# Kernel optimization log

Measured on AMD Instinct MI355X. Metric: run time of the kernel, lower is better.

Reference implementation:

```python
import jax, jax.numpy as jnp
import numpy as np

LN_EPS = 1e-5


def setup_inputs() -> dict:
    key = jax.random.key(0)
    kA, kX, kh = jax.random.split(key, 3)
    B, N, Cin, C, K = 16, 1024, 64, 64, 3
    A = jax.random.normal(kA, (B, N, N), dtype=jnp.float32)
    X = jax.random.normal(kX, (B, N, Cin), dtype=jnp.float32)
    h = jax.random.normal(kh, (K + 1, C, N), dtype=jnp.float32)
    ln_gamma = jnp.ones((C,), dtype=jnp.float32)
    ln_beta = jnp.zeros((C,), dtype=jnp.float32)
    return {"A": A, "X": X, "h": h, "ln_gamma": ln_gamma, "ln_beta": ln_beta}


def reference(A, X, h, ln_gamma, ln_beta):
    # Original loops compute, for each output channel c:
    #   sum_i sum_ch diag(h[i,c]) @ A^i @ X[..., ch]
    # which equals sum_i h[i,c,:] * (A^i @ X.sum(-1)).
    num_terms = h.shape[0] - 1  # static
    Xs = X.sum(-1)  # [B, N]
    powers = [Xs]
    p = Xs
    for _ in range(num_terms):  # static small loop over polynomial terms
        p = jnp.einsum('bnm,bm->bn', A, p)  # A^i @ Xs, matrix-vector per batch
        powers.append(p)
    P = jnp.stack(powers)  # [K+1, B, N]
    # node-variant per-channel taps: Y[b,n,c] = sum_i h[i,c,n] * P[i,b,n]
    Y = jnp.einsum('icn,ibn->bnc', h, P)  # [B, N, C]
    mu = Y.mean(axis=-1, keepdims=True)
    var = Y.var(axis=-1, keepdims=True)
    Yn = (Y - mu) / jnp.sqrt(var + LN_EPS) * ln_gamma + ln_beta
    return jnp.tanh(Yn)
```

## Files before the change

### kernel.cpp

```cpp
#include <hip/hip_runtime.h>
#include <math.h>

constexpr int B = 16, N = 1024, Cin = 64, C = 64, K = 3;
#define LN_EPS 1e-5f

__global__ void __launch_bounds__(256) k_front(const float* __restrict__ X,
                                               const float* __restrict__ h,
                                               float* __restrict__ P,
                                               float* __restrict__ ht) {
    __shared__ float tile[64 * 65];
    const int tid  = threadIdx.x;
    const int lane = tid & 63;
    const int w    = tid >> 6;
    const int gw   = blockIdx.x * 4 + w;

    for (int p = gw; p < B * N; p += 4096) {
        float v = X[(size_t)p * Cin + lane];
        #pragma unroll
        for (int off = 32; off; off >>= 1) v += __shfl_xor(v, off);
        if (lane == 0) P[p] = v;
    }

    if (blockIdx.x < (K + 1) * (N / 64)) {
        int i  = blockIdx.x / (N / 64);
        int n0 = (blockIdx.x % (N / 64)) * 64;
        const float* hi = h + (size_t)i * C * N;
        #pragma unroll
        for (int cc = w; cc < 64; cc += 4)
            tile[cc * 65 + lane] = hi[(size_t)cc * N + n0 + lane];
        __syncthreads();
        float* hti = ht + (size_t)i * N * C;
        #pragma unroll
        for (int nn = w; nn < 64; nn += 4)
            hti[(size_t)(n0 + nn) * C + lane] = tile[lane * 65 + nn];
    }
}

__device__ __forceinline__ void matvec4(const float* __restrict__ Ab,
                                        const float4* __restrict__ xs,
                                        int row, int lane,
                                        float& a0, float& a1, float& a2, float& a3) {
    const float4* r0 = (const float4*)(Ab + (size_t)(row + 0) * N);
    const float4* r1 = (const float4*)(Ab + (size_t)(row + 1) * N);
    const float4* r2 = (const float4*)(Ab + (size_t)(row + 2) * N);
    const float4* r3 = (const float4*)(Ab + (size_t)(row + 3) * N);
    a0 = a1 = a2 = a3 = 0.f;
    #pragma unroll
    for (int k = 0; k < 4; ++k) {
        int idx = k * 64 + lane;
        float4 xx = xs[idx];
        float4 v0 = r0[idx];
        float4 v1 = r1[idx];
        float4 v2 = r2[idx];
        float4 v3 = r3[idx];
        a0 += v0.x * xx.x + v0.y * xx.y + v0.z * xx.z + v0.w * xx.w;
        a1 += v1.x * xx.x + v1.y * xx.y + v1.z * xx.z + v1.w * xx.w;
        a2 += v2.x * xx.x + v2.y * xx.y + v2.z * xx.z + v2.w * xx.w;
        a3 += v3.x * xx.x + v3.y * xx.y + v3.z * xx.z + v3.w * xx.w;
    }
    #pragma unroll
    for (int off = 32; off; off >>= 1) {
        a0 += __shfl_xor(a0, off);
        a1 += __shfl_xor(a1, off);
        a2 += __shfl_xor(a2, off);
        a3 += __shfl_xor(a3, off);
    }
}

__global__ void __launch_bounds__(256) k_matvec(const float* __restrict__ A,
                                                const float* __restrict__ x,
                                                float* __restrict__ y) {
    __shared__ __align__(16) float4 xs[N / 4];
    const int b    = blockIdx.x >> 6;
    const int row0 = (blockIdx.x & 63) << 4;
    xs[threadIdx.x] = ((const float4*)(x + (size_t)b * N))[threadIdx.x];
    __syncthreads();

    const int w    = threadIdx.x >> 6;
    const int lane = threadIdx.x & 63;
    float a0, a1, a2, a3;
    matvec4(A + ((size_t)b << 20), xs, row0 + w * 4, lane, a0, a1, a2, a3);
    if (lane == 0) {
        float* yb = y + (size_t)b * N + row0 + w * 4;
        yb[0] = a0; yb[1] = a1; yb[2] = a2; yb[3] = a3;
    }
}

__global__ void __launch_bounds__(256) k_last(const float* __restrict__ A,
                                              const float* __restrict__ P,
                                              const float* __restrict__ ht,
                                              const float* __restrict__ gamma,
                                              const float* __restrict__ beta,
                                              float* __restrict__ out) {
    __shared__ __align__(16) float4 xs[N / 4];
    __shared__ float p3s[16];
    const int b    = blockIdx.x >> 6;
    const int row0 = (blockIdx.x & 63) << 4;
    const float* x2 = P + (size_t)2 * B * N + (size_t)b * N;
    xs[threadIdx.x] = ((const float4*)x2)[threadIdx.x];
    __syncthreads();

    const int w    = threadIdx.x >> 6;
    const int lane = threadIdx.x & 63;
    float a0, a1, a2, a3;
    matvec4(A + ((size_t)b << 20), xs, row0 + w * 4, lane, a0, a1, a2, a3);
    if (lane == 0) {
        p3s[w * 4 + 0] = a0; p3s[w * 4 + 1] = a1;
        p3s[w * 4 + 2] = a2; p3s[w * 4 + 3] = a3;
    }
    __syncthreads();

    const float g = gamma[lane];
    const float be = beta[lane];
    #pragma unroll
    for (int j = 0; j < 4; ++j) {
        const int nn = w * 4 + j;
        const int n  = row0 + nn;
        float y = 0.f;
        #pragma unroll
        for (int i = 0; i < 3; ++i) {
            float hv = ht[((size_t)i * N + n) * C + lane];
            float pv = P[(size_t)i * B * N + (size_t)b * N + n];
            y += hv * pv;
        }
        y += ht[((size_t)3 * N + n) * C + lane] * p3s[nn];
        float s = y;
        #pragma unroll
        for (int off = 32; off; off >>= 1) s += __shfl_xor(s, off);
        float mu = s * (1.0f / 64.0f);
        float d  = y - mu;
        float v  = d * d;
        #pragma unroll
        for (int off = 32; off; off >>= 1) v += __shfl_xor(v, off);
        float var = v * (1.0f / 64.0f);
        float yn  = d * rsqrtf(var + LN_EPS) * g + be;
        out[((size_t)b * N + n) * C + lane] = tanhf(yn);
    }
}

extern "C" void kernel_launch(void* const* d_in, const int* in_sizes, int n_in,
                              void* d_out, int out_size, void* d_ws, size_t ws_size,
                              hipStream_t stream) {
    const float* A     = (const float*)d_in[0];
    const float* X     = (const float*)d_in[1];
    const float* h     = (const float*)d_in[2];
    const float* gamma = (const float*)d_in[3];
    const float* beta  = (const float*)d_in[4];
    float* out = (float*)d_out;

    float* P  = (float*)d_ws;
    float* ht = P + (size_t)3 * B * N;

    k_front<<<1024, 256, 0, stream>>>(X, h, P, ht);
    k_matvec<<<B * (N / 16), 256, 0, stream>>>(A, P, P + (size_t)B * N);
    k_matvec<<<B * (N / 16), 256, 0, stream>>>(A, P + (size_t)B * N,
                                               P + (size_t)2 * B * N);
    k_last<<<B * (N / 16), 256, 0, stream>>>(A, P, ht, gamma, beta, out);
}
```

Baseline: 136.6 us.

## Fuse all stages into one persistent kernel with grid-wide atomic barriers

Replaces the four separate launches (front reduction/transpose, two matvecs, final matvec+layernorm) with a single persistent kernel of 512 blocks that syncs the stages through atomic counter barriers in workspace, reset by a memset each call. Each block now handles 32 rows per batch instead of 16. The aim is to remove per-launch overhead and the gaps between kernels. In exchange it relies on all 512 blocks being resident at once, and the spin barrier breaks out after a fixed count, which could silently give wrong results if blocks are not co-scheduled.

```diff
diff --git a/kernel.cpp b/kernel.cpp
--- a/kernel.cpp
+++ b/kernel.cpp
@@ -2,38 +2,22 @@
 #include <math.h>
 
 constexpr int B = 16, N = 1024, Cin = 64, C = 64, K = 3;
+constexpr int BN = B * N;
+constexpr int GRID = 512;
 #define LN_EPS 1e-5f
 
-__global__ void __launch_bounds__(256) k_front(const float* __restrict__ X,
-                                               const float* __restrict__ h,
-                                               float* __restrict__ P,
-                                               float* __restrict__ ht) {
-    __shared__ float tile[64 * 65];
-    const int tid  = threadIdx.x;
-    const int lane = tid & 63;
-    const int w    = tid >> 6;
-    const int gw   = blockIdx.x * 4 + w;
-
-    for (int p = gw; p < B * N; p += 4096) {
-        float v = X[(size_t)p * Cin + lane];
-        #pragma unroll
-        for (int off = 32; off; off >>= 1) v += __shfl_xor(v, off);
-        if (lane == 0) P[p] = v;
+__device__ __forceinline__ void gbar(unsigned int* cnt, unsigned int target) {
+    __threadfence();
+    __syncthreads();
+    if (threadIdx.x == 0) {
+        __hip_atomic_fetch_add(cnt, 1u, __ATOMIC_RELEASE, __HIP_MEMORY_SCOPE_AGENT);
+        int spins = 0;
+        while (__hip_atomic_load(cnt, __ATOMIC_ACQUIRE, __HIP_MEMORY_SCOPE_AGENT) < target) {
+            if (++spins > (1 << 20)) break;
+        }
     }
-
-    if (blockIdx.x < (K + 1) * (N / 64)) {
-        int i  = blockIdx.x / (N / 64);
-        int n0 = (blockIdx.x % (N / 64)) * 64;
-        const float* hi = h + (size_t)i * C * N;
-        #pragma unroll
-        for (int cc = w; cc < 64; cc += 4)
-            tile[cc * 65 + lane] = hi[(size_t)cc * N + n0 + lane];
-        __syncthreads();
-        float* hti = ht + (size_t)i * N * C;
-        #pragma unroll
-        for (int nn = w; nn < 64; nn += 4)
-            hti[(size_t)(n0 + nn) * C + lane] = tile[lane * 65 + nn];
-    }
+    __syncthreads();
+    __threadfence();
 }
 
 __device__ __forceinline__ void matvec4(const float* __restrict__ Ab,
@@ -67,74 +51,106 @@
     }
 }
 
-__global__ void __launch_bounds__(256) k_matvec(const float* __restrict__ A,
-                                                const float* __restrict__ x,
-                                                float* __restrict__ y) {
-    __shared__ __align__(16) float4 xs[N / 4];
-    const int b    = blockIdx.x >> 6;
-    const int row0 = (blockIdx.x & 63) << 4;
-    xs[threadIdx.x] = ((const float4*)(x + (size_t)b * N))[threadIdx.x];
-    __syncthreads();
+__global__ void __launch_bounds__(256)
+fused_persist(const float* __restrict__ A, const float* __restrict__ X,
+              const float* __restrict__ h, const float* __restrict__ gamma,
+              const float* __restrict__ beta, float* __restrict__ out,
+              unsigned int* __restrict__ bar, float* __restrict__ P,
+              float* __restrict__ ht) {
+    __shared__ __align__(16) float smem[64 * 65];
+    __shared__ float p3s[32];
+    const int tid  = threadIdx.x;
+    const int lane = tid & 63;
+    const int w    = tid >> 6;
+    const int gw   = blockIdx.x * 4 + w;
 
-    const int w    = threadIdx.x >> 6;
-    const int lane = threadIdx.x & 63;
-    float a0, a1, a2, a3;
-    matvec4(A + ((size_t)b << 20), xs, row0 + w * 4, lane, a0, a1, a2, a3);
-    if (lane == 0) {
-        float* yb = y + (size_t)b * N + row0 + w * 4;
-        yb[0] = a0; yb[1] = a1; yb[2] = a2; yb[3] = a3;
-    }
-}
-
-__global__ void __launch_bounds__(256) k_last(const float* __restrict__ A,
-                                              const float* __restrict__ P,
-                                              const float* __restrict__ ht,
-                                              const float* __restrict__ gamma,
-                                              const float* __restrict__ beta,
-                                              float* __restrict__ out) {
-    __shared__ __align__(16) float4 xs[N / 4];
-    __shared__ float p3s[16];
-    const int b    = blockIdx.x >> 6;
-    const int row0 = (blockIdx.x & 63) << 4;
-    const float* x2 = P + (size_t)2 * B * N + (size_t)b * N;
-    xs[threadIdx.x] = ((const float4*)x2)[threadIdx.x];
-    __syncthreads();
-
-    const int w    = threadIdx.x >> 6;
-    const int lane = threadIdx.x & 63;
-    float a0, a1, a2, a3;
-    matvec4(A + ((size_t)b << 20), xs, row0 + w * 4, lane, a0, a1, a2, a3);
-    if (lane == 0) {
-        p3s[w * 4 + 0] = a0; p3s[w * 4 + 1] = a1;
-        p3s[w * 4 + 2] = a2; p3s[w * 4 + 3] = a3;
-    }
-    __syncthreads();
-
-    const float g = gamma[lane];
-    const float be = beta[lane];
-    #pragma unroll
-    for (int j = 0; j < 4; ++j) {
-        const int nn = w * 4 + j;
-        const int n  = row0 + nn;
-        float y = 0.f;
-        #pragma unroll
-        for (int i = 0; i < 3; ++i) {
-            float hv = ht[((size_t)i * N + n) * C + lane];
-            float pv = P[(size_t)i * B * N + (size_t)b * N + n];
-            y += hv * pv;
-        }
-        y += ht[((size_t)3 * N + n) * C + lane] * p3s[nn];
-        float s = y;
-        #pragma unroll
-        for (int off = 32; off; off >>= 1) s += __shfl_xor(s, off);
-        float mu = s * (1.0f / 64.0f);
-        float d  = y - mu;
-        float v  = d * d;
+    for (int p = gw; p < BN; p += 4 * GRID) {
+        float v = X[(size_t)p * Cin + lane];
         #pragma unroll
         for (int off = 32; off; off >>= 1) v += __shfl_xor(v, off);
-        float var = v * (1.0f / 64.0f);
-        float yn  = d * rsqrtf(var + LN_EPS) * g + be;
-        out[((size_t)b * N + n) * C + lane] = tanhf(yn);
+        if (lane == 0) P[p] = v;
+    }
+
+    if (blockIdx.x < (K + 1) * (N / 64)) {
+        int i  = blockIdx.x / (N / 64);
+        int n0 = (blockIdx.x % (N / 64)) * 64;
+        const float* hi = h + (size_t)i * C * N;
+        #pragma unroll
+        for (int cc = w; cc < 64; cc += 4)
+            smem[cc * 65 + lane] = hi[(size_t)cc * N + n0 + lane];
+        __syncthreads();
+        float* hti = ht + (size_t)i * N * C;
+        #pragma unroll
+        for (int nn = w; nn < 64; nn += 4)
+            hti[(size_t)(n0 + nn) * C + lane] = smem[lane * 65 + nn];
+    }
+    gbar(bar + 0, GRID);
+
+    const int b     = blockIdx.x >> 5;
+    const int rbase = (blockIdx.x & 31) << 5;
+    const float* Ab = A + ((size_t)b << 20);
+    float4* xs = (float4*)smem;
+
+    for (int it = 0; it < 2; ++it) {
+        const float* xsrc = P + (size_t)it * BN + (size_t)b * N;
+        float* ydst       = P + (size_t)(it + 1) * BN + (size_t)b * N;
+        xs[tid] = ((const float4*)xsrc)[tid];
+        __syncthreads();
+        #pragma unroll
+        for (int r = 0; r < 2; ++r) {
+            const int row = rbase + r * 16 + w * 4;
+            float a0, a1, a2, a3;
+            matvec4(Ab, xs, row, lane, a0, a1, a2, a3);
+            if (lane == 0) {
+                float* yb = ydst + row;
+                yb[0] = a0; yb[1] = a1; yb[2] = a2; yb[3] = a3;
+            }
+        }
+        gbar(bar + 1 + it, GRID);
+    }
+
+    {
+        const float* xsrc = P + (size_t)2 * BN + (size_t)b * N;
+        xs[tid] = ((const float4*)xsrc)[tid];
+        __syncthreads();
+        #pragma unroll
+        for (int r = 0; r < 2; ++r) {
+            const int row = rbase + r * 16 + w * 4;
+            float a0, a1, a2, a3;
+            matvec4(Ab, xs, row, lane, a0, a1, a2, a3);
+            if (lane == 0) {
+                int o = r * 16 + w * 4;
+                p3s[o + 0] = a0; p3s[o + 1] = a1; p3s[o + 2] = a2; p3s[o + 3] = a3;
+            }
+        }
+        __syncthreads();
+
+        const float g  = gamma[lane];
+        const float be = beta[lane];
+        #pragma unroll
+        for (int j = 0; j < 8; ++j) {
+            const int nn = w * 8 + j;
+            const int n  = rbase + nn;
+            float y = 0.f;
+            #pragma unroll
+            for (int i = 0; i < 3; ++i) {
+                float hv = ht[((size_t)i * N + n) * C + lane];
+                float pv = P[(size_t)i * BN + (size_t)b * N + n];
+                y += hv * pv;
+            }
+            y += ht[((size_t)3 * N + n) * C + lane] * p3s[nn];
+            float s = y;
+            #pragma unroll
+            for (int off = 32; off; off >>= 1) s += __shfl_xor(s, off);
+            float mu = s * (1.0f / 64.0f);
+            float d  = y - mu;
+            float v  = d * d;
+            #pragma unroll
+            for (int off = 32; off; off >>= 1) v += __shfl_xor(v, off);
+            float var = v * (1.0f / 64.0f);
+            float yn  = d * rsqrtf(var + LN_EPS) * g + be;
+            out[((size_t)b * N + n) * C + lane] = tanhf(yn);
+        }
     }
 }
 
@@ -148,12 +164,10 @@
     const float* beta  = (const float*)d_in[4];
     float* out = (float*)d_out;
 
-    float* P  = (float*)d_ws;
-    float* ht = P + (size_t)3 * B * N;
+    unsigned int* bar = (unsigned int*)d_ws;
+    float* P  = (float*)d_ws + 64;
+    float* ht = P + (size_t)3 * BN;
 
-    k_front<<<1024, 256, 0, stream>>>(X, h, P, ht);
-    k_matvec<<<B * (N / 16), 256, 0, stream>>>(A, P, P + (size_t)B * N);
-    k_matvec<<<B * (N / 16), 256, 0, stream>>>(A, P + (size_t)B * N,
-                                               P + (size_t)2 * B * N);
-    k_last<<<B * (N / 16), 256, 0, stream>>>(A, P, ht, gamma, beta, out);
+    hipMemsetAsync(bar, 0, 64 * sizeof(unsigned int), stream);
+    fused_persist<<<GRID, 256, 0, stream>>>(A, X, h, gamma, beta, out, bar, P, ht);
 }
```

Result: slower. 505.1 us (+269.8%).
